# Performance work log

Measured on AMD Instinct MI355X. Metric: run time of the kernel, lower is better.

## Reference

```python
import jax, jax.numpy as jnp
import numpy as np

B, S, H, I = 4, 2048, 2048, 8192
LN_EPS = 1e-6  # DeepSpeed inference layer-norm epsilon


def setup_inputs() -> dict:
    key = jax.random.key(0)
    ks = jax.random.split(key, 10)
    return {
        "input": jax.random.normal(ks[0], (B, S, H), dtype=jnp.float32),
        "residual": jax.random.normal(ks[1], (B, S, H), dtype=jnp.float32),
        "residual_norm": jax.random.normal(ks[2], (B, S, H), dtype=jnp.float32),
        "bias": jax.random.normal(ks[3], (H,), dtype=jnp.float32) * 0.02,
        "gamma": jnp.ones((H,), dtype=jnp.float32) + jax.random.normal(ks[4], (H,), dtype=jnp.float32) * 0.02,
        "beta": jax.random.normal(ks[5], (H,), dtype=jnp.float32) * 0.02,
        "inter_w": jax.random.normal(ks[6], (H, I), dtype=jnp.float32) * 0.02,
        "inter_b": jax.random.normal(ks[7], (I,), dtype=jnp.float32) * 0.02,
        "output_w": jax.random.normal(ks[8], (I, H), dtype=jnp.float32) * 0.02,
        "output_b": jax.random.normal(ks[9], (H,), dtype=jnp.float32) * 0.02,
    }


def reference(input, residual, residual_norm, bias, gamma, beta,
              inter_w, inter_b, output_w, output_b):
    # --- mlp_gemm_func (pre-LN path, attn_nw is not None) ---
    # Fused: residual_add = attention_output + attention_bias + residual
    residual_add = input + residual + bias                    # [B,S,H]
    # LayerNorm over hidden dim
    mu = jnp.mean(residual_add, axis=-1, keepdims=True)
    var = jnp.mean(jnp.square(residual_add - mu), axis=-1, keepdims=True)
    ln = (residual_add - mu) * jax.lax.rsqrt(var + LN_EPS) * gamma + beta
    # GEMM + bias + GeLU, then second GEMM
    h = jax.nn.gelu(jnp.einsum("bsh,hi->bsi", ln, inter_w) + inter_b,
                    approximate=False)                        # [B,S,I]
    out = jnp.einsum("bsi,ih->bsh", h, output_w)              # [B,S,H]
    # --- residual_add_func (pre-LN, mlp_after_attn): mlp_out + residual_add + final_bias ---
    return out + residual_add + output_b
```

## Files before the change

### kernel.cpp

```cpp
#include <hip/hip_runtime.h>

typedef __attribute__((ext_vector_type(8))) __bf16 bf16x8;
typedef __attribute__((ext_vector_type(4))) float f32x4;

#define AS1(p) ((const __attribute__((address_space(1))) void*)(uintptr_t)(p))
#define AS3(p) ((__attribute__((address_space(3))) void*)(uint32_t)(uintptr_t)(p))
#define GLD16(gp, lp) __builtin_amdgcn_global_load_lds(AS1(gp), AS3(lp), 16, 0, 0)

static constexpr int Bb = 4, Ss = 2048, Hh = 2048, Ih = 8192;
static constexpr int Mm = Bb * Ss;

__device__ __forceinline__ float gelu_exact(float x) {
    return 0.5f * x * (1.0f + erff(x * 0.70710678118654752440f));
}

__global__ __launch_bounds__(256) void transpose_cvt(const float* __restrict__ src,
                                                     __bf16* __restrict__ dst,
                                                     int R, int C) {
    __shared__ float tile[32][33];
    const int tx = threadIdx.x, ty = threadIdx.y;
    const int cB = blockIdx.x * 32, rB = blockIdx.y * 32;
#pragma unroll
    for (int i = 0; i < 4; ++i)
        tile[ty + i * 8][tx] = src[(size_t)(rB + ty + i * 8) * C + cB + tx];
    __syncthreads();
#pragma unroll
    for (int i = 0; i < 4; ++i)
        dst[(size_t)(cB + ty + i * 8) * R + rB + tx] = (__bf16)tile[tx][ty + i * 8];
}

__global__ __launch_bounds__(256) void fused_ln(const float* __restrict__ input,
                                                const float* __restrict__ residual,
                                                const float* __restrict__ bias,
                                                const float* __restrict__ gamma,
                                                const float* __restrict__ beta,
                                                __bf16* __restrict__ lnb,
                                                __bf16* __restrict__ rab) {
    const int row = blockIdx.x;
    const int tid = threadIdx.x;
    const size_t base = (size_t)row * Hh;
    const int e = tid * 8;

    float4 x0 = *(const float4*)(input + base + e);
    float4 x1 = *(const float4*)(input + base + e + 4);
    float4 r0 = *(const float4*)(residual + base + e);
    float4 r1 = *(const float4*)(residual + base + e + 4);
    float4 b0 = *(const float4*)(bias + e);
    float4 b1 = *(const float4*)(bias + e + 4);

    float s[8];
    s[0] = x0.x + r0.x + b0.x; s[1] = x0.y + r0.y + b0.y;
    s[2] = x0.z + r0.z + b0.z; s[3] = x0.w + r0.w + b0.w;
    s[4] = x1.x + r1.x + b1.x; s[5] = x1.y + r1.y + b1.y;
    s[6] = x1.z + r1.z + b1.z; s[7] = x1.w + r1.w + b1.w;

    float sum = 0.f, sq = 0.f;
#pragma unroll
    for (int j = 0; j < 8; ++j) { sum += s[j]; sq += s[j] * s[j]; }
#pragma unroll
    for (int o = 32; o > 0; o >>= 1) {
        sum += __shfl_xor(sum, o);
        sq  += __shfl_xor(sq, o);
    }
    __shared__ float red[8];
    const int wv = tid >> 6, ln_ = tid & 63;
    if (ln_ == 0) { red[wv] = sum; red[4 + wv] = sq; }
    __syncthreads();
    sum = red[0] + red[1] + red[2] + red[3];
    sq  = red[4] + red[5] + red[6] + red[7];

    const float mu   = sum * (1.0f / Hh);
    const float var  = sq * (1.0f / Hh) - mu * mu;
    const float rstd = rsqrtf(var + 1e-6f);

    float4 g0 = *(const float4*)(gamma + e);
    float4 g1 = *(const float4*)(gamma + e + 4);
    float4 t0 = *(const float4*)(beta + e);
    float4 t1 = *(const float4*)(beta + e + 4);
    float g[8] = {g0.x, g0.y, g0.z, g0.w, g1.x, g1.y, g1.z, g1.w};
    float t[8] = {t0.x, t0.y, t0.z, t0.w, t1.x, t1.y, t1.z, t1.w};

    bf16x8 lv, rv;
#pragma unroll
    for (int j = 0; j < 8; ++j) {
        rv[j] = (__bf16)s[j];
        lv[j] = (__bf16)((s[j] - mu) * rstd * g[j] + t[j]);
    }
    *(bf16x8*)(lnb + base + e) = lv;
    *(bf16x8*)(rab + base + e) = rv;
}


__device__ __forceinline__ void ldA4(const char* p0, const char* p1, const int mhOff,
                                     bf16x8 (&af)[4][2]) {
#pragma unroll
    for (int m = 0; m < 4; ++m) {
        af[m][0] = *(const bf16x8*)(p0 + mhOff + m * 2048);
        af[m][1] = *(const bf16x8*)(p1 + mhOff + m * 2048);
    }
}
__device__ __forceinline__ void ldB2(const char* p0, const char* p1, const int nhOff,
                                     bf16x8 (&bf)[2][2]) {
#pragma unroll
    for (int n = 0; n < 2; ++n) {
        bf[n][0] = *(const bf16x8*)(p0 + nhOff + n * 2048);
        bf[n][1] = *(const bf16x8*)(p1 + nhOff + n * 2048);
    }
}
template <int MH, int NH>
__device__ __forceinline__ void mfmaQ(const bf16x8 (&a)[4][2], const bf16x8 (&b)[2][2],
                                      f32x4 (&acc)[8][4]) {
#pragma unroll
    for (int m = 0; m < 4; ++m)
#pragma unroll
        for (int n = 0; n < 2; ++n)
#pragma unroll
            for (int ks = 0; ks < 2; ++ks)
                acc[MH * 4 + m][NH * 2 + n] = __builtin_amdgcn_mfma_f32_16x16x32_bf16(
                    a[m][ks], b[n][ks], acc[MH * 4 + m][NH * 2 + n], 0, 0, 0);
}
__device__ __forceinline__ void stage2(const __bf16* src, __bf16* dst, const size_t row64) {
    GLD16(src, dst);
    GLD16(src + row64, dst + 4096);
}

#define LGK8 asm volatile("s_waitcnt lgkmcnt(8)" ::: "memory")
#define PHASE_MID                                         \
    __builtin_amdgcn_s_barrier();                         \
    asm volatile("s_waitcnt lgkmcnt(0)" ::: "memory");    \
    __builtin_amdgcn_s_setprio(1)
#define PHASE_END                                         \
    __builtin_amdgcn_s_setprio(0);                        \
    __builtin_amdgcn_s_barrier()

template <int MODE>
__global__ __launch_bounds__(512, 2) void gemm256(const __bf16* __restrict__ A,
                                                  const __bf16* __restrict__ Bt,
                                                  const float* __restrict__ bias,
                                                  const __bf16* __restrict__ rab,
                                                  __bf16* __restrict__ outH,
                                                  float* __restrict__ outF,
                                                  int M, int N, int K) {
    __shared__ __align__(128) __bf16 lds[2 * 4 * 128 * 64];

    const int tid = threadIdx.x;
    const int nbx = N >> 8;
    const int nwg = gridDim.x;
    const int cpx = nwg >> 3;
    const int bid = blockIdx.x;
    const int swz = (bid & 7) * cpx + (bid >> 3);
    const int by = swz / nbx, bx = swz - by * nbx;
    const int mBase = by << 8, nBase = bx << 8;

    const int wave = tid >> 6, lane = tid & 63;
    const int wr = wave >> 2, wc = wave & 3;

    const int NT = K >> 6;
    const int NI = NT >> 1;

    char* ldsc = (char*)lds;
    const int laneCol0 = (((lane >> 4) << 4)) ^ ((lane & 7) << 4);
    const int laneCol1 = laneCol0 ^ 64;
    const int aLaneR = (lane & 15) << 7;
    const int bLaneR = (((wc & 1) << 6) + (lane & 15)) << 7;
    const char* pA[2][2] = {
        {ldsc + (0 * 4 + wr) * 16384 + aLaneR + laneCol0,
         ldsc + (0 * 4 + wr) * 16384 + aLaneR + laneCol1},
        {ldsc + (1 * 4 + wr) * 16384 + aLaneR + laneCol0,
         ldsc + (1 * 4 + wr) * 16384 + aLaneR + laneCol1}};
    const char* pB[2][2] = {
        {ldsc + (0 * 4 + 2 + (wc >> 1)) * 16384 + bLaneR + laneCol0,
         ldsc + (0 * 4 + 2 + (wc >> 1)) * 16384 + bLaneR + laneCol1},
        {ldsc + (1 * 4 + 2 + (wc >> 1)) * 16384 + bLaneR + laneCol0,
         ldsc + (1 * 4 + 2 + (wc >> 1)) * 16384 + bLaneR + laneCol1}};

    const int srow = tid >> 3;
    const int scol = ((tid & 7) ^ (srow & 7)) << 3;
    const __bf16* aSt = A + (size_t)(mBase + srow) * K + scol;
    const __bf16* bSt = Bt + (size_t)(nBase + srow) * K + scol;
    __bf16* lw = lds + tid * 8;
    const size_t row64 = (size_t)64 * K;
    const size_t row128 = (size_t)128 * K;

#define STA(buf, h, t) stage2(aSt + (h) * row128 + (size_t)(t) * 64, lw + ((buf) * 4 + (h)) * 8192, row64)
#define STB(buf, h, t) stage2(bSt + (h) * row128 + (size_t)(t) * 64, lw + ((buf) * 4 + 2 + (h)) * 8192, row64)

    f32x4 acc[8][4] = {};
    bf16x8 af[4][2], b0[2][2], b1[2][2];

    STA(0, 0, 0); STA(0, 1, 0); STB(0, 0, 0); STB(0, 1, 0);
    STB(1, 0, 1); STB(1, 1, 1);
    asm volatile("s_waitcnt vmcnt(4)" ::: "memory");
    __builtin_amdgcn_s_barrier();

    for (int i = 0; i < NI; ++i) {
        const int t0 = 2 * i, t1 = 2 * i + 1;
        const bool pf0 = (t0 + 2 < NT);
        const bool pf1 = (t1 + 2 < NT);

        ldA4(pA[0][0], pA[0][1], 0, af);
        ldB2(pB[0][0], pB[0][1], 0, b0);
        STA(1, 0, t1);
        LGK8;
        PHASE_MID; mfmaQ<0, 0>(af, b0, acc); PHASE_END;

        ldB2(pB[0][0], pB[0][1], 4096, b1);
        STA(1, 1, t1);
        PHASE_MID; mfmaQ<0, 1>(af, b1, acc); PHASE_END;

        ldA4(pA[0][0], pA[0][1], 8192, af);
        if (pf0) STB(0, 0, t0 + 2);
        PHASE_MID; mfmaQ<1, 1>(af, b1, acc); PHASE_END;

        if (pf0) STB(0, 1, t0 + 2);
        PHASE_MID; mfmaQ<1, 0>(af, b0, acc);
        __builtin_amdgcn_s_setprio(0);
        if (pf0) { asm volatile("s_waitcnt vmcnt(4)" ::: "memory"); }
        else     { asm volatile("s_waitcnt vmcnt(0)" ::: "memory"); }
        __builtin_amdgcn_s_barrier();

        ldA4(pA[1][0], pA[1][1], 0, af);
        ldB2(pB[1][0], pB[1][1], 0, b0);
        if (pf0) STA(0, 0, t0 + 2);
        LGK8;
        PHASE_MID; mfmaQ<0, 0>(af, b0, acc); PHASE_END;

        ldB2(pB[1][0], pB[1][1], 4096, b1);
        if (pf0) STA(0, 1, t0 + 2);
        PHASE_MID; mfmaQ<0, 1>(af, b1, acc); PHASE_END;

        ldA4(pA[1][0], pA[1][1], 8192, af);
        if (pf1) STB(1, 0, t1 + 2);
        PHASE_MID; mfmaQ<1, 1>(af, b1, acc); PHASE_END;

        if (pf1) STB(1, 1, t1 + 2);
        PHASE_MID; mfmaQ<1, 0>(af, b0, acc);
        __builtin_amdgcn_s_setprio(0);
        if (pf1) { asm volatile("s_waitcnt vmcnt(4)" ::: "memory"); }
        __builtin_amdgcn_s_barrier();
    }

    const int r0 = mBase + wr * 128 + ((lane >> 4) << 2);
    const int c0 = nBase + wc * 64 + (lane & 15);
    float bb[4];
#pragma unroll
    for (int nf = 0; nf < 4; ++nf) bb[nf] = bias[c0 + nf * 16];
#pragma unroll
    for (int mf = 0; mf < 8; ++mf) {
        const int row = r0 + mf * 16;
#pragma unroll
        for (int nf = 0; nf < 4; ++nf) {
            const int col = c0 + nf * 16;
#pragma unroll
            for (int j = 0; j < 4; ++j) {
                const size_t idx = (size_t)(row + j) * N + col;
                const float v = acc[mf][nf][j] + bb[nf];
                if (MODE == 0) {
                    outH[idx] = (__bf16)gelu_exact(v);
                } else {
                    outF[idx] = v + (float)rab[idx];
                }
            }
        }
    }
#undef STA
#undef STB
}

extern "C" void kernel_launch(void* const* d_in, const int* in_sizes, int n_in,
                              void* d_out, int out_size, void* d_ws, size_t ws_size,
                              hipStream_t stream) {
    const float* input    = (const float*)d_in[0];
    const float* residual = (const float*)d_in[1];
    const float* bias     = (const float*)d_in[3];
    const float* gamma    = (const float*)d_in[4];
    const float* beta     = (const float*)d_in[5];
    const float* inter_w  = (const float*)d_in[6];
    const float* inter_b  = (const float*)d_in[7];
    const float* output_w = (const float*)d_in[8];
    const float* output_b = (const float*)d_in[9];
    float* out = (float*)d_out;

    __bf16* w1t  = (__bf16*)d_ws;
    __bf16* w2t  = w1t + (size_t)Ih * Hh;
    __bf16* lnb  = w2t + (size_t)Hh * Ih;
    __bf16* rab  = lnb + (size_t)Mm * Hh;
    __bf16* hbuf = rab + (size_t)Mm * Hh;

    transpose_cvt<<<dim3(Ih / 32, Hh / 32), dim3(32, 8), 0, stream>>>(inter_w, w1t, Hh, Ih);
    transpose_cvt<<<dim3(Hh / 32, Ih / 32), dim3(32, 8), 0, stream>>>(output_w, w2t, Ih, Hh);

    fused_ln<<<Mm, 256, 0, stream>>>(input, residual, bias, gamma, beta, lnb, rab);

    gemm256<0><<<dim3((Mm / 256) * (Ih / 256)), 512, 0, stream>>>(
        lnb, w1t, inter_b, nullptr, hbuf, nullptr, Mm, Ih, Hh);

    gemm256<1><<<dim3((Mm / 256) * (Hh / 256)), 512, 0, stream>>>(
        hbuf, w2t, output_b, rab, nullptr, out, Mm, Hh, Ih);
}
```

Before: 611.9 us.

## Restructure GEMM main loop to overlap LDS reads with MFMA phases

Reorganizes the software pipeline in the 256x256 bf16 GEMM main loop so each MFMA quadrant runs immediately, with the LDS fragment reads for the next quadrant and the global-to-LDS stages issued after it. This cuts the barrier count per quadrant from two to one and drops the explicit lgkmcnt waits, so MFMA work can hide LDS latency. The vmcnt waits are moved to finer points. The ordering of barriers relative to the async LDS writes now depends on compiler-inserted waits, which risks both correctness races and stalls.

```diff
diff --git a/kernel.cpp b/kernel.cpp
--- a/kernel.cpp
+++ b/kernel.cpp
@@ -91,20 +91,27 @@
 }
 
 
-__device__ __forceinline__ void ldA4(const char* p0, const char* p1, const int mhOff,
-                                     bf16x8 (&af)[4][2]) {
+#define CFENCE asm volatile("" ::: "memory")
+#define BARX   do { CFENCE; __builtin_amdgcn_s_barrier(); CFENCE; } while (0)
+#define SP1 __builtin_amdgcn_s_setprio(1)
+#define SP0 __builtin_amdgcn_s_setprio(0)
+#define VM2 asm volatile("s_waitcnt vmcnt(2)" ::: "memory")
+#define VM0 asm volatile("s_waitcnt vmcnt(0)" ::: "memory")
+
+__device__ __forceinline__ void rdA(bf16x8 (&af)[4][2], const char* p0, const char* p1,
+                                    const int off) {
 #pragma unroll
     for (int m = 0; m < 4; ++m) {
-        af[m][0] = *(const bf16x8*)(p0 + mhOff + m * 2048);
-        af[m][1] = *(const bf16x8*)(p1 + mhOff + m * 2048);
-    }
-}
-__device__ __forceinline__ void ldB2(const char* p0, const char* p1, const int nhOff,
-                                     bf16x8 (&bf)[2][2]) {
+        af[m][0] = *(const bf16x8*)(p0 + off + m * 2048);
+        af[m][1] = *(const bf16x8*)(p1 + off + m * 2048);
+    }
+}
+__device__ __forceinline__ void rdB(bf16x8 (&bf)[2][2], const char* p0, const char* p1,
+                                    const int off) {
 #pragma unroll
     for (int n = 0; n < 2; ++n) {
-        bf[n][0] = *(const bf16x8*)(p0 + nhOff + n * 2048);
-        bf[n][1] = *(const bf16x8*)(p1 + nhOff + n * 2048);
+        bf[n][0] = *(const bf16x8*)(p0 + off + n * 2048);
+        bf[n][1] = *(const bf16x8*)(p1 + off + n * 2048);
     }
 }
 template <int MH, int NH>
@@ -123,15 +130,6 @@
     GLD16(src, dst);
     GLD16(src + row64, dst + 4096);
 }
-
-#define LGK8 asm volatile("s_waitcnt lgkmcnt(8)" ::: "memory")
-#define PHASE_MID                                         \
-    __builtin_amdgcn_s_barrier();                         \
-    asm volatile("s_waitcnt lgkmcnt(0)" ::: "memory");    \
-    __builtin_amdgcn_s_setprio(1)
-#define PHASE_END                                         \
-    __builtin_amdgcn_s_setprio(0);                        \
-    __builtin_amdgcn_s_barrier()
 
 template <int MODE>
 __global__ __launch_bounds__(512, 2) void gemm256(const __bf16* __restrict__ A,
@@ -189,55 +187,52 @@
     bf16x8 af[4][2], b0[2][2], b1[2][2];
 
     STA(0, 0, 0); STA(0, 1, 0); STB(0, 0, 0); STB(0, 1, 0);
+    VM0;
+    BARX;
     STB(1, 0, 1); STB(1, 1, 1);
-    asm volatile("s_waitcnt vmcnt(4)" ::: "memory");
-    __builtin_amdgcn_s_barrier();
+    rdA(af, pA[0][0], pA[0][1], 0);
+    rdB(b0, pB[0][0], pB[0][1], 0);
 
     for (int i = 0; i < NI; ++i) {
         const int t0 = 2 * i, t1 = 2 * i + 1;
         const bool pf0 = (t0 + 2 < NT);
         const bool pf1 = (t1 + 2 < NT);
-
-        ldA4(pA[0][0], pA[0][1], 0, af);
-        ldB2(pB[0][0], pB[0][1], 0, b0);
+        const bool last = (i == NI - 1);
+
+        SP1; mfmaQ<0, 0>(af, b0, acc); SP0;
+        rdB(b1, pB[0][0], pB[0][1], 4096);
         STA(1, 0, t1);
-        LGK8;
-        PHASE_MID; mfmaQ<0, 0>(af, b0, acc); PHASE_END;
-
-        ldB2(pB[0][0], pB[0][1], 4096, b1);
+        BARX;
+        SP1; mfmaQ<0, 1>(af, b1, acc); SP0;
+        rdA(af, pA[0][0], pA[0][1], 8192);
         STA(1, 1, t1);
-        PHASE_MID; mfmaQ<0, 1>(af, b1, acc); PHASE_END;
-
-        ldA4(pA[0][0], pA[0][1], 8192, af);
-        if (pf0) STB(0, 0, t0 + 2);
-        PHASE_MID; mfmaQ<1, 1>(af, b1, acc); PHASE_END;
-
+        BARX;
+        SP1; mfmaQ<1, 1>(af, b1, acc); SP0;
+        if (pf0) { STB(0, 0, t0 + 2); VM2; } else { VM0; }
+        BARX;
+        SP1; mfmaQ<1, 0>(af, b0, acc); SP0;
+        rdA(af, pA[1][0], pA[1][1], 0);
+        rdB(b0, pB[1][0], pB[1][1], 0);
         if (pf0) STB(0, 1, t0 + 2);
-        PHASE_MID; mfmaQ<1, 0>(af, b0, acc);
-        __builtin_amdgcn_s_setprio(0);
-        if (pf0) { asm volatile("s_waitcnt vmcnt(4)" ::: "memory"); }
-        else     { asm volatile("s_waitcnt vmcnt(0)" ::: "memory"); }
-        __builtin_amdgcn_s_barrier();
-
-        ldA4(pA[1][0], pA[1][1], 0, af);
-        ldB2(pB[1][0], pB[1][1], 0, b0);
+        BARX;
+        SP1; mfmaQ<0, 0>(af, b0, acc); SP0;
+        rdB(b1, pB[1][0], pB[1][1], 4096);
         if (pf0) STA(0, 0, t0 + 2);
-        LGK8;
-        PHASE_MID; mfmaQ<0, 0>(af, b0, acc); PHASE_END;
-
-        ldB2(pB[1][0], pB[1][1], 4096, b1);
+        BARX;
+        SP1; mfmaQ<0, 1>(af, b1, acc); SP0;
+        rdA(af, pA[1][0], pA[1][1], 8192);
         if (pf0) STA(0, 1, t0 + 2);
-        PHASE_MID; mfmaQ<0, 1>(af, b1, acc); PHASE_END;
-
-        ldA4(pA[1][0], pA[1][1], 8192, af);
-        if (pf1) STB(1, 0, t1 + 2);
-        PHASE_MID; mfmaQ<1, 1>(af, b1, acc); PHASE_END;
-
+        BARX;
+        SP1; mfmaQ<1, 1>(af, b1, acc); SP0;
+        if (pf1) { STB(1, 0, t1 + 2); VM2; } else { VM0; }
+        BARX;
+        SP1; mfmaQ<1, 0>(af, b0, acc); SP0;
+        if (!last) {
+            rdA(af, pA[0][0], pA[0][1], 0);
+            rdB(b0, pB[0][0], pB[0][1], 0);
+        }
         if (pf1) STB(1, 1, t1 + 2);
-        PHASE_MID; mfmaQ<1, 0>(af, b0, acc);
-        __builtin_amdgcn_s_setprio(0);
-        if (pf1) { asm volatile("s_waitcnt vmcnt(4)" ::: "memory"); }
-        __builtin_amdgcn_s_barrier();
+        BARX;
     }
 
     const int r0 = mBase + wr * 128 + ((lane >> 4) << 2);
```

Result: faster. 592.9 us (-3.1%).
